# Kernel optimization log

Hardware: AMD Instinct MI355X
Metric: run time of the kernel (lower is better)

## Reference

```python
import jax, jax.numpy as jnp
import numpy as np

B, X, Y, Z = 2, 64, 64, 48
T_IN, T_OUT = 10, 20
WIDTH = 20
G = 4              # number of fields / groups
M1 = M2 = M3 = 8   # fourier modes
L = 4              # layers
ORDER = [[0, 1, 2, 3], [1, 2, 3, 0], [2, 3, 0, 1], [3, 0, 1, 2]]
CIN = WIDTH * 4    # mWidth_input_parameters[i] == 4
COUT = WIDTH       # nWidth_output_parameters[i] == 1
EPS = 1e-5


def setup_inputs() -> dict:
    key = jax.random.key(0)
    ks = jax.random.split(key, 12)
    s = 0.02
    return {
        "x": jax.random.normal(ks[0], (B, X, Y, Z, G * T_IN), jnp.float32),
        "p_w": jax.random.normal(ks[1], (G, T_IN + 3, WIDTH), jnp.float32) * s,
        "p_b": jnp.zeros((G, WIDTH), jnp.float32),
        # complex spectral weights stored as (..., 2) = (real, imag); 4 corner blocks
        "spec_w": jax.random.normal(ks[2], (L, G, 4, CIN, COUT, M1, M2, M3, 2), jnp.float32) * (1.0 / CIN),
        "mlp_w1": jax.random.normal(ks[3], (L, G, COUT, COUT), jnp.float32) * s,
        "mlp_b1": jnp.zeros((L, G, COUT), jnp.float32),
        "mlp_w2": jax.random.normal(ks[4], (L, G, COUT, COUT), jnp.float32) * s,
        "mlp_b2": jnp.zeros((L, G, COUT), jnp.float32),
        "w_w": jax.random.normal(ks[5], (L, G, COUT, CIN), jnp.float32) * s,
        "w_b": jnp.zeros((L, G, COUT), jnp.float32),
        "q_w1": jax.random.normal(ks[6], (G, 4 * COUT, COUT), jnp.float32) * s,
        "q_b1": jnp.zeros((G, 4 * COUT), jnp.float32),
        "q_w2": jax.random.normal(ks[7], (G, T_OUT, 4 * COUT), jnp.float32) * s,
        "q_b2": jnp.zeros((G, T_OUT), jnp.float32),
    }


def _instance_norm(v):  # (B,C,X,Y,Z); InstanceNorm3d, affine=False
    m = v.mean(axis=(-3, -2, -1), keepdims=True)
    var = v.var(axis=(-3, -2, -1), keepdims=True)
    return (v - m) * jax.lax.rsqrt(var + EPS)


def _conv1x1(v, w, b):  # w: (Co, Ci)
    return jnp.einsum('bixyz,oi->boxyz', v, w) + b[None, :, None, None, None]


def _gelu(v):
    return jax.nn.gelu(v, approximate=False)


def _spectral(v, w):  # v: (B,Ci,X,Y,Z); w: complex (4,Ci,Co,M1,M2,M3)
    ft = jnp.fft.rfftn(v, axes=(-3, -2, -1))
    mul = lambda xc, wc: jnp.einsum('bixyz,ioxyz->boxyz', xc, wc)
    out = jnp.zeros((v.shape[0], w.shape[2], X, Y, Z // 2 + 1), ft.dtype)
    out = out.at[:, :, :M1, :M2, :M3].set(mul(ft[:, :, :M1, :M2, :M3], w[0]))
    out = out.at[:, :, -M1:, :M2, :M3].set(mul(ft[:, :, -M1:, :M2, :M3], w[1]))
    out = out.at[:, :, :M1, -M2:, :M3].set(mul(ft[:, :, :M1, -M2:, :M3], w[2]))
    out = out.at[:, :, -M1:, -M2:, :M3].set(mul(ft[:, :, -M1:, -M2:, :M3], w[3]))
    return jnp.fft.irfftn(out, s=(X, Y, Z), axes=(-3, -2, -1))


def _grid():  # (1,X,Y,Z,3), linspace 0..1 per axis
    gx = jnp.linspace(0.0, 1.0, X, dtype=jnp.float32)[:, None, None]
    gy = jnp.linspace(0.0, 1.0, Y, dtype=jnp.float32)[None, :, None]
    gz = jnp.linspace(0.0, 1.0, Z, dtype=jnp.float32)[None, None, :]
    g = jnp.stack([jnp.broadcast_to(gx, (X, Y, Z)),
                   jnp.broadcast_to(gy, (X, Y, Z)),
                   jnp.broadcast_to(gz, (X, Y, Z))], axis=-1)
    return g[None]


def reference(x, p_w, p_b, spec_w, mlp_w1, mlp_b1, mlp_w2, mlp_b2,
              w_w, w_b, q_w1, q_b1, q_w2, q_b2):
    grid = jnp.broadcast_to(_grid(), (x.shape[0], X, Y, Z, 3))
    # --- lifting: per-field Linear(T_in+3 -> width) ---
    lifted = [jnp.concatenate([x[..., i * T_IN:(i + 1) * T_IN], grid], axis=-1) @ p_w[i] + p_b[i]
              for i in range(G)]
    h = jnp.concatenate(lifted, axis=-1).transpose(0, 4, 1, 2, 3)  # (B, width*G, X, Y, Z)
    sw = spec_w[..., 0] + 1j * spec_w[..., 1]
    for l in range(L):
        for i in range(G):
            # faithful gather quirk: first index duplicated, last index dropped
            idx = [ORDER[i][0]] + ORDER[i][:-1]
            xg = jnp.concatenate([h[:, WIDTH * k:WIDTH * (k + 1)] for k in idx], axis=1)
            v = _instance_norm(xg)
            v = _spectral(v, sw[l, i])
            v = _instance_norm(v)
            v = _conv1x1(_gelu(_conv1x1(v, mlp_w1[l, i], mlp_b1[l, i])), mlp_w2[l, i], mlp_b2[l, i])
            r = _conv1x1(xg, w_w[l, i], w_b[l, i])
            h = h.at[:, WIDTH * i:WIDTH * (i + 1)].set(v + r)
        if l != L - 1:
            h = _gelu(h)
    # --- projection: per-field MLP (T_OUT == WIDTH so slices align to field blocks) ---
    outs = []
    for i in range(G):
        lo = (WIDTH if i == 0 else T_OUT) * i
        xi = h[:, lo:lo + WIDTH]
        xi = _conv1x1(_gelu(_conv1x1(xi, q_w1[i], q_b1[i])), q_w2[i], q_b2[i])
        outs.append(xi)
    out = jnp.concatenate(outs, axis=1)
    return out.transpose(0, 2, 3, 4, 1)  # (B,X,Y,Z,G*T_OUT)
```

## Files before the change

### kernel.cpp

```cpp
#include <hip/hip_runtime.h>
#include <math.h>

#define SPAT 196608
#define EPSV 1e-5f

__device__ __forceinline__ float geluf(float x){
    float ax = fabsf(x)*0.70710678118654752440f;
    float t = __builtin_amdgcn_rcpf(1.0f + 0.3275911f*ax);
    float p = ((((1.061405429f*t - 1.453152027f)*t + 1.421413741f)*t - 0.284496736f)*t + 0.254829592f)*t;
    float e = 1.0f - p*__expf(-ax*ax);
    float er = copysignf(e, x);
    return 0.5f*x*(1.0f + er);
}
__device__ __forceinline__ float wred(float v){
    #pragma unroll
    for(int o=32;o>0;o>>=1) v += __shfl_down(v,o);
    return v;
}

__global__ void k_tables(float* tab){
    for(int idx=threadIdx.x; idx<384; idx+=blockDim.x){
        int z = idx>>3, k = idx&7;
        double a = 6.283185307179586476925286766559 * (double)((k*z)%48) / 48.0;
        float c = (float)cos(a), s = (float)sin(a);
        tab[idx]=c; tab[384+idx]=s;
        tab[768 + k*48+z]=c; tab[1152 + k*48+z]=s;
    }
    for(int idx=threadIdx.x; idx<1024; idx+=blockDim.x){
        int y = idx>>4, ki = idx&15;
        int ka = ki<8 ? ki : ki+48;
        double a = 6.283185307179586476925286766559 * (double)((ka*y)%64) / 64.0;
        float c=(float)cos(a), s=(float)sin(a);
        tab[1536+idx]=c; tab[2560+idx]=s;
        tab[3584 + ki*64+y]=c; tab[4608 + ki*64+y]=s;
    }
}

__global__ void __launch_bounds__(256) k_lift(const float* __restrict__ x,
                       const float* __restrict__ pw, const float* __restrict__ pb,
                       float* __restrict__ h){
    int t = blockIdx.x*256 + threadIdx.x;
    int b = (t>=SPAT) ? 1 : 0; int col = t - b*SPAT;
    int xy = col/48, z = col%48;
    const float4* xp = (const float4*)(x + (size_t)t*40);
    float in[40];
    #pragma unroll
    for(int q=0;q<10;q++){
        float4 v = xp[q];
        in[q*4]=v.x; in[q*4+1]=v.y; in[q*4+2]=v.z; in[q*4+3]=v.w;
    }
    float gx = (float)(xy>>6)*(1.0f/63.0f);
    float gy = (float)(xy&63)*(1.0f/63.0f);
    float gz = (float)z*(1.0f/47.0f);
    for(int g=0;g<4;g++){
        const float* w = pw + g*260;
        #pragma unroll 4
        for(int c=0;c<20;c++){
            float a = pb[g*20+c];
            #pragma unroll
            for(int j=0;j<10;j++) a += in[g*10+j]*w[j*20+c];
            a += gx*w[200+c] + gy*w[220+c] + gz*w[240+c];
            h[(size_t)(b*80+g*20+c)*SPAT + col] = a;
        }
    }
}

__global__ void __launch_bounds__(256) k_zy(const float* __restrict__ h,
        float* __restrict__ ybuf, float* __restrict__ partZY,
        const float* __restrict__ tab, int gA,int gB,int gC,int gD, int gflag){
    __shared__ float sp4[4*16*65];
    __shared__ float cyl[16*65], syl[16*65];
    __shared__ float sred[8];
    int blk = blockIdx.x;
    int x = blk&63; int d=(blk>>6)%20; int r2 = blk/1280; int b = r2&1; int gi = r2>>1;
    int gl4[4]={gA,gB,gC,gD};
    int g = gl4[gi];
    int ch = g*20+d;
    int tid=threadIdx.x;
    int y = tid&63, q4 = tid>>6;
    const float4* src = (const float4*)(h + (size_t)(b*80+ch)*SPAT + (size_t)x*3072
                                          + (size_t)(y*48 + q4*12));
    float v[12];
    #pragma unroll
    for(int u=0;u<3;u++){
        float4 t4 = src[u];
        v[u*4]=t4.x; v[u*4+1]=t4.y; v[u*4+2]=t4.z; v[u*4+3]=t4.w;
    }
    if(gflag){
        #pragma unroll
        for(int j=0;j<12;j++) v[j]=geluf(v[j]);
    }
    float s1=0,s2=0;
    #pragma unroll
    for(int j=0;j<12;j++){ s1+=v[j]; s2+=v[j]*v[j]; }
    for(int tt=tid;tt<1024;tt+=256){
        int ki=tt>>6, yy=tt&63;
        cyl[ki*65+yy]=tab[3584+tt]; syl[ki*65+yy]=tab[4608+tt];
    }
    const float* CZ = tab+768  + q4*12;
    const float* SZ = tab+1152 + q4*12;
    #pragma unroll
    for(int k=0;k<8;k++){
        float rr=0, si=0;
        #pragma unroll
        for(int j=0;j<12;j++){ rr += v[j]*CZ[k*48+j]; si += v[j]*SZ[k*48+j]; }
        sp4[(q4*16 + k*2)*65 + y]   = rr;
        sp4[(q4*16 + k*2+1)*65 + y] = -si;
    }
    s1=wred(s1); s2=wred(s2);
    if((tid&63)==0){ sred[(tid>>6)*2]=s1; sred[(tid>>6)*2+1]=s2; }
    __syncthreads();
    if(tid==0){
        size_t pi = ((size_t)(b*80+ch)*64+x)*2;
        partZY[pi]   = sred[0]+sred[2]+sred[4]+sred[6];
        partZY[pi+1] = sred[1]+sred[3]+sred[5]+sred[7];
    }
    #pragma unroll
    for(int j=0;j<4;j++){
        int e = tid + j*256;
        int kri = e>>6, yy = e&63;
        float sum = sp4[kri*65+yy] + sp4[(16+kri)*65+yy]
                  + sp4[(32+kri)*65+yy] + sp4[(48+kri)*65+yy];
        sp4[kri*65+yy] = sum;
    }
    __syncthreads();
    if(tid<128){
        int ky=tid>>3, kz=tid&7;
        const float* cy = cyl+ky*65; const float* sy = syl+ky*65;
        const float* spr = sp4 + (kz*2)*65;
        const float* spi = sp4 + (kz*2+1)*65;
        float fr=0, fi=0;
        #pragma unroll 8
        for(int yy=0;yy<64;yy++){
            float sr=spr[yy], si=spi[yy];
            float c=cy[yy], s=sy[yy];
            fr += sr*c + si*s;
            fi += si*c - sr*s;
        }
        size_t base = ((size_t)((g*2+b)*20+d)*16 + ky)*1024 + (size_t)(kz*128);
        ybuf[base + x]      = fr;
        ybuf[base + 64 + x] = fi;
    }
}

__global__ void __launch_bounds__(128) k_xdft(const float* __restrict__ ybuf,
        float* __restrict__ fbufC, const float* __restrict__ partZY,
        const float* __restrict__ tab, int gA,int gB,int gC,int gD){
    __shared__ __align__(16) float ylx[16*68];
    __shared__ float cxl[16*65], sxl[16*65];
    __shared__ float scs[1];
    int blk = blockIdx.x;
    int kyi = blk&15; int d=(blk>>4)%20; int r2=blk/320; int b=r2&1; int gi=r2>>1;
    int gl4[4]={gA,gB,gC,gD};
    int g=gl4[gi]; int ch=g*20+d;
    int tid=threadIdx.x;
    const float4* src = (const float4*)(ybuf + (((size_t)((g*2+b)*20+d)*16+kyi)*1024));
    #pragma unroll
    for(int u=0;u<2;u++){
        int e=tid+u*128; float4 v=src[e];
        int kzri = e>>4; int xx=(e&15)*4;
        *(float4*)(ylx + kzri*68 + xx) = v;
    }
    for(int tt=tid;tt<1024;tt+=128){
        int ki=tt>>6, y=tt&63;
        cxl[ki*65+y]=tab[3584+tt]; sxl[ki*65+y]=tab[4608+tt];
    }
    float s1=0,s2=0;
    if(tid<64){
        size_t pi=((size_t)(b*80+ch)*64+tid)*2;
        s1=partZY[pi]; s2=partZY[pi+1];
    }
    s1=wred(s1); s2=wred(s2);
    if(tid==0){
        float mean=s1*(1.0f/196608.0f);
        float var=s2*(1.0f/196608.0f)-mean*mean;
        scs[0]=rsqrtf(var+EPSV);
    }
    __syncthreads();
    float sc = scs[0];
    int kxi=tid>>3, kz=tid&7;
    const float* yr = ylx + (kz*2)*68;
    const float* yi = ylx + (kz*2+1)*68;
    const float* cx = cxl + kxi*65;
    const float* sx = sxl + kxi*65;
    float fr=0, fi=0;
    #pragma unroll 8
    for(int xx=0;xx<64;xx++){
        float a=yr[xx], e2=yi[xx];
        float c=cx[xx], s=sx[xx];
        fr += a*c + e2*s;
        fi += e2*c - a*s;
    }
    fr*=sc; fi*=sc;
    if(kxi==0 && kyi==0 && kz==0){ fr=0.0f; fi=0.0f; }
    size_t idx = ((size_t)(b*80+ch)*2048 + (size_t)((kxi*16+kyi)*8+kz))*2;
    fbufC[idx]=fr; fbufC[idx+1]=fi;
}

__global__ void __launch_bounds__(256) k_spec(const float* __restrict__ fbufC,
        const float* __restrict__ sw, float* __restrict__ gbuf,
        float* __restrict__ stat2, int li, int g0, int g1, int g2){
    __shared__ float part[2112];
    int blk = blockIdx.x;
    int m1p = blk & 3, o = (blk>>2)%20, q = blk/80;
    int tid = threadIdx.x;
    int t64 = tid & 63, cc = tid >> 6;
    if(q==0 && m1p==0 && tid<2){
        stat2[(tid*20+o)*2]=0.f; stat2[(tid*20+o)*2+1]=0.f;
    }
    int offx = (q&1)*8, offy = (q>>1)*8;
    int m1 = m1p*2 + (t64>>5);
    int m2 = (t64>>2)&7;
    int m3 = (t64&3)*2;
    int tw = m1*64 + m2*8 + m3;
    int kxi = m1+offx, kyi = m2+offy;
    int fo = (kxi*16 + kyi)*8 + m3;
    const float4* wp = (const float4*)(sw + (((size_t)(li*4+q)*1600) + o)*1024 + (size_t)tw*2);
    const float4* fb = (const float4*)fbufC + (fo>>1);
    float r00=0,i00=0,r01=0,i01=0, r10=0,i10=0,r11=0,i11=0;
    int c0 = cc*5;
    #pragma unroll
    for(int u=0;u<5;u++){
        int c = c0+u;
        float4 wa = wp[(size_t)c*5120];
        float4 wb4= wp[(size_t)(c+20)*5120];
        float wr0 = wa.x + wb4.x, wi0 = wa.y + wb4.y, wr1 = wa.z + wb4.z, wi1 = wa.w + wb4.w;
        float4 f0 = fb[(size_t)(g0*20+c)*1024];
        float4 f1 = fb[(size_t)(80+g0*20+c)*1024];
        r00 += f0.x*wr0 - f0.y*wi0; i00 += f0.x*wi0 + f0.y*wr0;
        r01 += f0.z*wr1 - f0.w*wi1; i01 += f0.z*wi1 + f0.w*wr1;
        r10 += f1.x*wr0 - f1.y*wi0; i10 += f1.x*wi0 + f1.y*wr0;
        r11 += f1.z*wr1 - f1.w*wi1; i11 += f1.z*wi1 + f1.w*wr1;
    }
    #pragma unroll
    for(int u=0;u<5;u++){
        int c = c0+u;
        float4 wa = wp[(size_t)(c+40)*5120];
        float4 f0 = fb[(size_t)(g1*20+c)*1024];
        float4 f1 = fb[(size_t)(80+g1*20+c)*1024];
        r00 += f0.x*wa.x - f0.y*wa.y; i00 += f0.x*wa.y + f0.y*wa.x;
        r01 += f0.z*wa.z - f0.w*wa.w; i01 += f0.z*wa.w + f0.w*wa.z;
        r10 += f1.x*wa.x - f1.y*wa.y; i10 += f1.x*wa.y + f1.y*wa.x;
        r11 += f1.z*wa.z - f1.w*wa.w; i11 += f1.z*wa.w + f1.w*wa.z;
    }
    #pragma unroll
    for(int u=0;u<5;u++){
        int c = c0+u;
        float4 wa = wp[(size_t)(c+60)*5120];
        float4 f0 = fb[(size_t)(g2*20+c)*1024];
        float4 f1 = fb[(size_t)(80+g2*20+c)*1024];
        r00 += f0.x*wa.x - f0.y*wa.y; i00 += f0.x*wa.y + f0.y*wa.x;
        r01 += f0.z*wa.z - f0.w*wa.w; i01 += f0.z*wa.w + f0.w*wa.z;
        r10 += f1.x*wa.x - f1.y*wa.y; i10 += f1.x*wa.y + f1.y*wa.x;
        r11 += f1.z*wa.z - f1.w*wa.w; i11 += f1.z*wa.w + f1.w*wa.z;
    }
    float vals[8]={r00,i00,r01,i01,r10,i10,r11,i11};
    #pragma unroll
    for(int e=0;e<8;e++) part[t64*33 + e*4 + cc] = vals[e];
    __syncthreads();
    if(cc==0){
        float acc[8];
        #pragma unroll
        for(int e=0;e<8;e++){
            const float* p = part + t64*33 + e*4;
            acc[e] = p[0]+p[1]+p[2]+p[3];
        }
        float4* gg0 = (float4*)(gbuf + (size_t)o*4096 + fo*2);
        float4* gg1 = (float4*)(gbuf + (size_t)(20+o)*4096 + fo*2);
        *gg0 = make_float4(acc[0],acc[1],acc[2],acc[3]);
        *gg1 = make_float4(acc[4],acc[5],acc[6],acc[7]);
    }
}

__global__ void k_inv(const float* __restrict__ gbuf, float* __restrict__ iybuf,
                      float* __restrict__ stat2, const float* __restrict__ tab){
    __shared__ __align__(16) float gl[4096];
    __shared__ float tmp[256];
    __shared__ float cl[1088], sl[1088];
    __shared__ float ig[4];
    int blk = blockIdx.x;
    int nx = blk&63, o = (blk>>6)%20, b = blk/1280;
    const float4* src4 = (const float4*)(gbuf + (size_t)(b*20+o)*4096);
    for(int t=threadIdx.x;t<1024;t+=blockDim.x) ((float4*)gl)[t]=src4[t];
    for(int t=threadIdx.x;t<1024;t+=blockDim.x){
        int y=t>>4, ki=t&15;
        cl[y*17+ki]=tab[1536+t]; sl[y*17+ki]=tab[2560+t];
    }
    __syncthreads();
    {
        int kyi = threadIdx.x>>3, kz = threadIdx.x&7;
        float ar=0, ai=0;
        #pragma unroll 4
        for(int kxi=0;kxi<16;kxi++){
            float gr = gl[((kxi*16+kyi)*8+kz)*2], gi2 = gl[((kxi*16+kyi)*8+kz)*2+1];
            float c = cl[nx*17+kxi], s = sl[nx*17+kxi];
            ar += gr*c - gi2*s;
            ai += gi2*c + gr*s;
        }
        tmp[threadIdx.x*2]   = ar*(1.0f/64.0f);
        tmp[threadIdx.x*2+1] = ai*(1.0f/64.0f);
    }
    __syncthreads();
    float p1=0,p2=0;
    for(int j=0;j<4;j++){
        int out = threadIdx.x + j*128;
        int ny = out>>3, kz = out&7;
        float ar=0, ai=0;
        #pragma unroll 4
        for(int kyi=0;kyi<16;kyi++){
            float vr = tmp[(kyi*8+kz)*2], vi = tmp[(kyi*8+kz)*2+1];
            float c = cl[ny*17+kyi], s = sl[ny*17+kyi];
            ar += vr*c - vi*s;
            ai += vi*c + vr*s;
        }
        ar *= (1.0f/64.0f); ai *= (1.0f/64.0f);
        size_t idx = ((((size_t)(b*20+o)*64+nx)*64+ny)*8+kz)*2;
        iybuf[idx]=ar; iybuf[idx+1]=ai;
        if(kz==0){ p1 += ar; p2 += ar*ar; }
        else p2 += 2.0f*(ar*ar+ai*ai);
    }
    p2 *= (1.0f/48.0f);
    float r1=wred(p1), r2=wred(p2);
    int wv = threadIdx.x>>6;
    if((threadIdx.x&63)==0){ ig[wv*2]=r1; ig[wv*2+1]=r2; }
    __syncthreads();
    if(threadIdx.x==0){
        atomicAdd(&stat2[(b*20+o)*2],   ig[0]+ig[2]);
        atomicAdd(&stat2[(b*20+o)*2+1], ig[1]+ig[3]);
    }
}

__global__ void __launch_bounds__(256) k_passD(
        const float* __restrict__ iybuf,
        const float* __restrict__ w1, const float* __restrict__ b1,
        const float* __restrict__ w2, const float* __restrict__ b2,
        const float* __restrict__ ww, const float* __restrict__ wb,
        float* __restrict__ h,
        const float* __restrict__ stat2, const float* __restrict__ tab,
        int li, int grp, int g1, int g2, int f0, int f1, int f2){
    __shared__ __align__(16) float dl[2560];
    __shared__ float m2l[20], s2l[20];
    __shared__ float czl[384], szl[384];
    int blk = blockIdx.x;
    int nyt = blk&7, nx=(blk>>3)&63, b = blk>>9;
    int tid = threadIdx.x;
    for(int u=tid; u<640; u+=256){
        int o = u>>5, j = u&31;
        const float4* s4 = (const float4*)(iybuf + ((((size_t)(b*20+o)*64+nx)*64 + nyt*8)*16));
        ((float4*)dl)[o*32+j] = s4[j];
    }
    if(tid<20){
        float S1 = stat2[(b*20+tid)*2], S2 = stat2[(b*20+tid)*2+1];
        float mean = S1*(1.0f/196608.0f);
        float var = S2*(1.0f/196608.0f) - mean*mean;
        m2l[tid]=mean; s2l[tid]=rsqrtf(var+EPSV);
    }
    for(int t=tid;t<384;t+=256){ czl[t]=tab[768+t]; szl[t]=tab[1152+t]; }
    __syncthreads();
    if(tid>=192) return;
    int p0 = tid*2;
    int nyl = p0/48, nz0 = p0 - nyl*48;
    float vj0[20], vj1[20];
    #pragma unroll
    for(int o=0;o<20;o++){
        const float* dd = dl + o*128 + nyl*16;
        float a0 = dd[0], a1 = dd[0];
        #pragma unroll
        for(int k=1;k<8;k++){
            float dr = dd[k*2], di = dd[k*2+1];
            a0 += 2.0f*(dr*czl[k*48+nz0]   - di*szl[k*48+nz0]);
            a1 += 2.0f*(dr*czl[k*48+nz0+1] - di*szl[k*48+nz0+1]);
        }
        vj0[o] = (a0*(1.0f/48.0f) - m2l[o])*s2l[o];
        vj1[o] = (a1*(1.0f/48.0f) - m2l[o])*s2l[o];
    }
    const float* W1 = w1 + li*400; const float* W2 = w2 + li*400;
    const float* B1 = b1 + li*20;  const float* B2 = b2 + li*20;
    float t10[20], t11[20];
    #pragma unroll
    for(int oo=0;oo<20;oo++){
        float a0=B1[oo], a1=a0;
        #pragma unroll
        for(int j=0;j<20;j++){ float w=W1[oo*20+j]; a0+=vj0[j]*w; a1+=vj1[j]*w; }
        t10[oo]=geluf(a0); t11[oo]=geluf(a1);
    }
    float o0[20], o1[20];
    #pragma unroll
    for(int oo=0;oo<20;oo++){
        float a0=B2[oo], a1=a0;
        #pragma unroll
        for(int j=0;j<20;j++){ float w=W2[oo*20+j]; a0+=t10[j]*w; a1+=t11[j]*w; }
        o0[oo]=a0; o1[oo]=a1;
    }
    int sb = (nx*64 + nyt*8)*48;
    const float* W = ww + li*1600;
    const float* hb = h + (size_t)(b*80)*SPAT + sb + p0;
    #pragma unroll
    for(int o=0;o<20;o++){ float bv=wb[li*20+o]; o0[o]+=bv; o1[o]+=bv; }
    for(int c=0;c<20;c++){
        float2 vv = *(const float2*)(hb + (size_t)(grp*20+c)*SPAT);
        if(f0){ vv.x=geluf(vv.x); vv.y=geluf(vv.y); }
        #pragma unroll
        for(int o=0;o<20;o++){
            float w = W[o*80+c] + W[o*80+20+c];
            o0[o]+=w*vv.x; o1[o]+=w*vv.y;
        }
    }
    for(int c=0;c<20;c++){
        float2 vv = *(const float2*)(hb + (size_t)(g1*20+c)*SPAT);
        if(f1){ vv.x=geluf(vv.x); vv.y=geluf(vv.y); }
        #pragma unroll
        for(int o=0;o<20;o++){
            float w = W[o*80+40+c];
            o0[o]+=w*vv.x; o1[o]+=w*vv.y;
        }
    }
    for(int c=0;c<20;c++){
        float2 vv = *(const float2*)(hb + (size_t)(g2*20+c)*SPAT);
        if(f2){ vv.x=geluf(vv.x); vv.y=geluf(vv.y); }
        #pragma unroll
        for(int o=0;o<20;o++){
            float w = W[o*80+60+c];
            o0[o]+=w*vv.x; o1[o]+=w*vv.y;
        }
    }
    #pragma unroll
    for(int o=0;o<20;o++)
        *(float2*)(h + (size_t)(b*80+grp*20+o)*SPAT + sb + p0) = make_float2(o0[o],o1[o]);
}

__global__ void __launch_bounds__(256) k_head(const float* __restrict__ h,
        const float* __restrict__ qw1, const float* __restrict__ qb1,
        const float* __restrict__ qw2, const float* __restrict__ qb2,
        float* __restrict__ out){
    int g = blockIdx.x & 3;
    int t = (blockIdx.x>>2)*256 + threadIdx.x;
    if(t >= 196608) return;
    int b = (t>=98304) ? 1 : 0; int col = (t - b*98304)*2;
    const float* hb = h + (size_t)(b*80+g*20)*SPAT + col;
    float2 in20[20];
    #pragma unroll
    for(int j=0;j<20;j++) in20[j] = *(const float2*)(hb + (size_t)j*SPAT);
    float2 o20[20];
    #pragma unroll
    for(int o2=0;o2<20;o2++){ float bv = qb2[g*20+o2]; o20[o2].x=bv; o20[o2].y=bv; }
    for(int o8=0;o8<80;o8++){
        float bv = qb1[g*80+o8];
        float a0 = bv, a1 = bv;
        #pragma unroll
        for(int j=0;j<20;j++){
            float w = qw1[g*1600 + o8*20 + j];
            a0 += in20[j].x*w; a1 += in20[j].y*w;
        }
        a0 = geluf(a0); a1 = geluf(a1);
        #pragma unroll
        for(int o2=0;o2<20;o2++){
            float w = qw2[g*1600 + o2*80 + o8];
            o20[o2].x += a0*w; o20[o2].y += a1*w;
        }
    }
    float* op0 = out + ((size_t)(b*SPAT)+col)*80 + g*20;
    float* op1 = op0 + 80;
    #pragma unroll
    for(int q2=0;q2<5;q2++){
        *(float4*)(op0 + q2*4) = make_float4(o20[q2*4].x,o20[q2*4+1].x,o20[q2*4+2].x,o20[q2*4+3].x);
        *(float4*)(op1 + q2*4) = make_float4(o20[q2*4].y,o20[q2*4+1].y,o20[q2*4+2].y,o20[q2*4+3].y);
    }
}

extern "C" void kernel_launch(void* const* d_in, const int* in_sizes, int n_in,
                              void* d_out, int out_size, void* d_ws, size_t ws_size,
                              hipStream_t stream){
    (void)in_sizes; (void)n_in; (void)out_size;
    const float* x    = (const float*)d_in[0];
    const float* p_w  = (const float*)d_in[1];
    const float* p_b  = (const float*)d_in[2];
    const float* spec = (const float*)d_in[3];
    const float* w1   = (const float*)d_in[4];
    const float* b1   = (const float*)d_in[5];
    const float* w2   = (const float*)d_in[6];
    const float* b2   = (const float*)d_in[7];
    const float* ww   = (const float*)d_in[8];
    const float* wb   = (const float*)d_in[9];
    const float* qw1  = (const float*)d_in[10];
    const float* qb1  = (const float*)d_in[11];
    const float* qw2  = (const float*)d_in[12];
    const float* qb2  = (const float*)d_in[13];
    float* out = (float*)d_out;
    float* ws  = (float*)d_ws;

    if(ws_size < (size_t)37545552*4) return;

    float* h      = ws;
    float* ybuf   = ws + 31457280;
    float* gbuf   = ws + 34078720;
    float* iyb    = ws + 34242560;
    float* fbufC  = ws + 36864000;
    float* partZY = ws + 37519360;
    float* stat2  = ws + 37539840;
    float* tab    = ws + 37539920;

    k_tables<<<1,256,0,stream>>>(tab);
    k_lift<<<1536,256,0,stream>>>(x, p_w, p_b, h);

    static const int ORD3[4][3] = {{0,1,2},{1,2,3},{2,3,0},{3,0,1}};
    for(int l=0;l<4;l++){
        int lf = (l>0)?1:0;
        for(int bi=0;bi<2;bi++){
            if(bi==0){
                k_zy  <<<10240,256,0,stream>>>(h, ybuf, partZY, tab, 0,1,2,3, lf);
                k_xdft<<< 2560,128,0,stream>>>(ybuf, fbufC, partZY, tab, 0,1,2,3);
            } else {
                k_zy  <<< 5120,256,0,stream>>>(h, ybuf, partZY, tab, 0,1,0,0, 0);
                k_xdft<<< 1280,128,0,stream>>>(ybuf, fbufC, partZY, tab, 0,1,0,0);
            }
            for(int ii=0;ii<2;ii++){
                int i = bi*2+ii; int li = l*4+i;
                int g0=ORD3[i][0], g1=ORD3[i][1], g2=ORD3[i][2];
                (void)g0;
                int f0 = lf;
                int f1 = (g1<i)?0:lf;
                int f2 = (g2<i)?0:lf;
                k_spec <<< 320,256,0,stream>>>(fbufC, spec, gbuf, stat2, li, i, g1, g2);
                k_inv  <<<2560,128,0,stream>>>(gbuf, iyb, stat2, tab);
                k_passD<<<1024,256,0,stream>>>(iyb, w1, b1, w2, b2, ww, wb, h, stat2, tab,
                                               li, i, g1, g2, f0, f1, f2);
            }
        }
    }
    k_head<<<3072,256,0,stream>>>(h, qw1, qb1, qw2, qb2, out);
}
```

Measured before the change: 3.269 ms.

## Batch two field groups per spectral, inverse and pointwise pass

The spectral-multiply, inverse-DFT and pointwise MLP/residual kernels now each handle two independent field groups in a single launch instead of two. Workspace buffers for gbuf, iybuf and stats are doubled and indexed by group. The fused pointwise kernel reads each input field block of h once and feeds both groups' residual convolutions, which cuts repeated global reads and launch count. The cost is much higher register pressure from four 20-wide accumulator arrays plus larger shared memory, which may lower occupancy or cause spills.

```diff
diff --git a/kernel.cpp b/kernel.cpp
--- a/kernel.cpp
+++ b/kernel.cpp
@@ -197,16 +197,22 @@
     fbufC[idx]=fr; fbufC[idx+1]=fi;
 }
 
-__global__ void __launch_bounds__(256) k_spec(const float* __restrict__ fbufC,
+__global__ void __launch_bounds__(256) k_spec2(const float* __restrict__ fbufC,
         const float* __restrict__ sw, float* __restrict__ gbuf,
-        float* __restrict__ stat2, int li, int g0, int g1, int g2){
+        float* __restrict__ stat2, int li0,
+        int i0, int gA1, int gA2, int i1, int gB1, int gB2){
     __shared__ float part[2112];
     int blk = blockIdx.x;
-    int m1p = blk & 3, o = (blk>>2)%20, q = blk/80;
+    int it = blk/320; int r = blk - it*320;
+    int m1p = r & 3, o = (r>>2)%20, q = r/80;
+    int li = li0 + it;
+    int g0 = it ? i1 : i0;
+    int g1 = it ? gB1 : gA1;
+    int g2 = it ? gB2 : gA2;
     int tid = threadIdx.x;
     int t64 = tid & 63, cc = tid >> 6;
     if(q==0 && m1p==0 && tid<2){
-        stat2[(tid*20+o)*2]=0.f; stat2[(tid*20+o)*2+1]=0.f;
+        stat2[((it*2+tid)*20+o)*2]=0.f; stat2[((it*2+tid)*20+o)*2+1]=0.f;
     }
     int offx = (q&1)*8, offy = (q>>1)*8;
     int m1 = m1p*2 + (t64>>5);
@@ -265,22 +271,24 @@
             const float* p = part + t64*33 + e*4;
             acc[e] = p[0]+p[1]+p[2]+p[3];
         }
-        float4* gg0 = (float4*)(gbuf + (size_t)o*4096 + fo*2);
-        float4* gg1 = (float4*)(gbuf + (size_t)(20+o)*4096 + fo*2);
+        float* gb = gbuf + (size_t)it*163840;
+        float4* gg0 = (float4*)(gb + (size_t)o*4096 + fo*2);
+        float4* gg1 = (float4*)(gb + (size_t)(20+o)*4096 + fo*2);
         *gg0 = make_float4(acc[0],acc[1],acc[2],acc[3]);
         *gg1 = make_float4(acc[4],acc[5],acc[6],acc[7]);
     }
 }
 
-__global__ void k_inv(const float* __restrict__ gbuf, float* __restrict__ iybuf,
-                      float* __restrict__ stat2, const float* __restrict__ tab){
+__global__ void k_inv2(const float* __restrict__ gbuf, float* __restrict__ iybuf,
+                       float* __restrict__ stat2, const float* __restrict__ tab){
     __shared__ __align__(16) float gl[4096];
     __shared__ float tmp[256];
     __shared__ float cl[1088], sl[1088];
     __shared__ float ig[4];
     int blk = blockIdx.x;
-    int nx = blk&63, o = (blk>>6)%20, b = blk/1280;
-    const float4* src4 = (const float4*)(gbuf + (size_t)(b*20+o)*4096);
+    int it = blk/2560; int r = blk - it*2560;
+    int nx = r&63, o = (r>>6)%20, b = r/1280;
+    const float4* src4 = (const float4*)(gbuf + (size_t)it*163840 + (size_t)(b*20+o)*4096);
     for(int t=threadIdx.x;t<1024;t+=blockDim.x) ((float4*)gl)[t]=src4[t];
     for(int t=threadIdx.x;t<1024;t+=blockDim.x){
         int y=t>>4, ki=t&15;
@@ -314,7 +322,7 @@
             ai += vi*c + vr*s;
         }
         ar *= (1.0f/64.0f); ai *= (1.0f/64.0f);
-        size_t idx = ((((size_t)(b*20+o)*64+nx)*64+ny)*8+kz)*2;
+        size_t idx = ((((size_t)((it*2+b)*20+o)*64+nx)*64+ny)*8+kz)*2;
         iybuf[idx]=ar; iybuf[idx+1]=ai;
         if(kz==0){ p1 += ar; p2 += ar*ar; }
         else p2 += 2.0f*(ar*ar+ai*ai);
@@ -325,108 +333,152 @@
     if((threadIdx.x&63)==0){ ig[wv*2]=r1; ig[wv*2+1]=r2; }
     __syncthreads();
     if(threadIdx.x==0){
-        atomicAdd(&stat2[(b*20+o)*2],   ig[0]+ig[2]);
-        atomicAdd(&stat2[(b*20+o)*2+1], ig[1]+ig[3]);
-    }
-}
-
-__global__ void __launch_bounds__(256) k_passD(
+        atomicAdd(&stat2[((it*2+b)*20+o)*2],   ig[0]+ig[2]);
+        atomicAdd(&stat2[((it*2+b)*20+o)*2+1], ig[1]+ig[3]);
+    }
+}
+
+__global__ void __launch_bounds__(256) k_passD2(
         const float* __restrict__ iybuf,
         const float* __restrict__ w1, const float* __restrict__ b1,
         const float* __restrict__ w2, const float* __restrict__ b2,
         const float* __restrict__ ww, const float* __restrict__ wb,
         float* __restrict__ h,
         const float* __restrict__ stat2, const float* __restrict__ tab,
-        int li, int grp, int g1, int g2, int f0, int f1, int f2){
-    __shared__ __align__(16) float dl[2560];
-    __shared__ float m2l[20], s2l[20];
+        int li0, int i0, int i1, int gA1, int gA2, int gB1, int gB2,
+        int fl0, int fl1, int fl2, int fl3){
+    __shared__ __align__(16) float dl[5120];
+    __shared__ float m2l[2][20], s2l[2][20];
     __shared__ float czl[384], szl[384];
     int blk = blockIdx.x;
     int nyt = blk&7, nx=(blk>>3)&63, b = blk>>9;
     int tid = threadIdx.x;
-    for(int u=tid; u<640; u+=256){
-        int o = u>>5, j = u&31;
-        const float4* s4 = (const float4*)(iybuf + ((((size_t)(b*20+o)*64+nx)*64 + nyt*8)*16));
-        ((float4*)dl)[o*32+j] = s4[j];
-    }
-    if(tid<20){
-        float S1 = stat2[(b*20+tid)*2], S2 = stat2[(b*20+tid)*2+1];
+    for(int u=tid; u<1280; u+=256){
+        int itu = (u>=640)?1:0; int rem = u - itu*640;
+        int o = rem>>5, j = rem&31;
+        const float4* s4 = (const float4*)(iybuf +
+            ((((size_t)((itu*2+b)*20+o)*64+nx)*64 + nyt*8)*16));
+        ((float4*)dl)[itu*640 + o*32 + j] = s4[j];
+    }
+    if(tid<40){
+        int itq = tid/20, oq = tid - itq*20;
+        float S1 = stat2[((itq*2+b)*20+oq)*2], S2 = stat2[((itq*2+b)*20+oq)*2+1];
         float mean = S1*(1.0f/196608.0f);
         float var = S2*(1.0f/196608.0f) - mean*mean;
-        m2l[tid]=mean; s2l[tid]=rsqrtf(var+EPSV);
+        m2l[itq][oq]=mean; s2l[itq][oq]=rsqrtf(var+EPSV);
     }
     for(int t=tid;t<384;t+=256){ czl[t]=tab[768+t]; szl[t]=tab[1152+t]; }
     __syncthreads();
     if(tid>=192) return;
     int p0 = tid*2;
     int nyl = p0/48, nz0 = p0 - nyl*48;
-    float vj0[20], vj1[20];
+    float oA0[20], oA1[20], oB0[20], oB1[20];
+    {
+        float vj0[20], vj1[20];
+        #pragma unroll
+        for(int o=0;o<20;o++){
+            const float* dd = dl + o*128 + nyl*16;
+            float a0 = dd[0], a1 = dd[0];
+            #pragma unroll
+            for(int k=1;k<8;k++){
+                float dr = dd[k*2], di = dd[k*2+1];
+                a0 += 2.0f*(dr*czl[k*48+nz0]   - di*szl[k*48+nz0]);
+                a1 += 2.0f*(dr*czl[k*48+nz0+1] - di*szl[k*48+nz0+1]);
+            }
+            vj0[o] = (a0*(1.0f/48.0f) - m2l[0][o])*s2l[0][o];
+            vj1[o] = (a1*(1.0f/48.0f) - m2l[0][o])*s2l[0][o];
+        }
+        const float* W1 = w1 + li0*400; const float* W2 = w2 + li0*400;
+        const float* B1 = b1 + li0*20;  const float* B2 = b2 + li0*20;
+        float t10[20], t11[20];
+        #pragma unroll
+        for(int oo=0;oo<20;oo++){
+            float a0=B1[oo], a1=a0;
+            #pragma unroll
+            for(int j=0;j<20;j++){ float w=W1[oo*20+j]; a0+=vj0[j]*w; a1+=vj1[j]*w; }
+            t10[oo]=geluf(a0); t11[oo]=geluf(a1);
+        }
+        #pragma unroll
+        for(int oo=0;oo<20;oo++){
+            float bb = B2[oo] + wb[li0*20+oo];
+            float a0=bb, a1=bb;
+            #pragma unroll
+            for(int j=0;j<20;j++){ float w=W2[oo*20+j]; a0+=t10[j]*w; a1+=t11[j]*w; }
+            oA0[oo]=a0; oA1[oo]=a1;
+        }
+    }
+    {
+        int li1 = li0+1;
+        float vj0[20], vj1[20];
+        #pragma unroll
+        for(int o=0;o<20;o++){
+            const float* dd = dl + 2560 + o*128 + nyl*16;
+            float a0 = dd[0], a1 = dd[0];
+            #pragma unroll
+            for(int k=1;k<8;k++){
+                float dr = dd[k*2], di = dd[k*2+1];
+                a0 += 2.0f*(dr*czl[k*48+nz0]   - di*szl[k*48+nz0]);
+                a1 += 2.0f*(dr*czl[k*48+nz0+1] - di*szl[k*48+nz0+1]);
+            }
+            vj0[o] = (a0*(1.0f/48.0f) - m2l[1][o])*s2l[1][o];
+            vj1[o] = (a1*(1.0f/48.0f) - m2l[1][o])*s2l[1][o];
+        }
+        const float* W1 = w1 + li1*400; const float* W2 = w2 + li1*400;
+        const float* B1 = b1 + li1*20;  const float* B2 = b2 + li1*20;
+        float t10[20], t11[20];
+        #pragma unroll
+        for(int oo=0;oo<20;oo++){
+            float a0=B1[oo], a1=a0;
+            #pragma unroll
+            for(int j=0;j<20;j++){ float w=W1[oo*20+j]; a0+=vj0[j]*w; a1+=vj1[j]*w; }
+            t10[oo]=geluf(a0); t11[oo]=geluf(a1);
+        }
+        #pragma unroll
+        for(int oo=0;oo<20;oo++){
+            float bb = B2[oo] + wb[li1*20+oo];
+            float a0=bb, a1=bb;
+            #pragma unroll
+            for(int j=0;j<20;j++){ float w=W2[oo*20+j]; a0+=t10[j]*w; a1+=t11[j]*w; }
+            oB0[oo]=a0; oB1[oo]=a1;
+        }
+    }
+    int sb = (nx*64 + nyt*8)*48;
+    const float* hb = h + (size_t)(b*80)*SPAT + sb + p0;
+    const float* WA = ww + li0*1600;
+    const float* WB = ww + (li0+1)*1600;
+    #pragma unroll
+    for(int g=0; g<4; g++){
+        int flag = (g==0)?fl0:((g==1)?fl1:((g==2)?fl2:fl3));
+        for(int c=0;c<20;c++){
+            float2 vv = *(const float2*)(hb + (size_t)(g*20+c)*SPAT);
+            if(flag){ vv.x=geluf(vv.x); vv.y=geluf(vv.y); }
+            if(g==i0){
+                #pragma unroll
+                for(int o=0;o<20;o++){ float w = WA[o*80+c]+WA[o*80+20+c]; oA0[o]+=w*vv.x; oA1[o]+=w*vv.y; }
+            } else if(g==gA1){
+                #pragma unroll
+                for(int o=0;o<20;o++){ float w = WA[o*80+40+c]; oA0[o]+=w*vv.x; oA1[o]+=w*vv.y; }
+            } else if(g==gA2){
+                #pragma unroll
+                for(int o=0;o<20;o++){ float w = WA[o*80+60+c]; oA0[o]+=w*vv.x; oA1[o]+=w*vv.y; }
+            }
+            if(g==i1){
+                #pragma unroll
+                for(int o=0;o<20;o++){ float w = WB[o*80+c]+WB[o*80+20+c]; oB0[o]+=w*vv.x; oB1[o]+=w*vv.y; }
+            } else if(g==gB1){
+                #pragma unroll
+                for(int o=0;o<20;o++){ float w = WB[o*80+40+c]; oB0[o]+=w*vv.x; oB1[o]+=w*vv.y; }
+            } else if(g==gB2){
+                #pragma unroll
+                for(int o=0;o<20;o++){ float w = WB[o*80+60+c]; oB0[o]+=w*vv.x; oB1[o]+=w*vv.y; }
+            }
+        }
+    }
     #pragma unroll
     for(int o=0;o<20;o++){
-        const float* dd = dl + o*128 + nyl*16;
-        float a0 = dd[0], a1 = dd[0];
-        #pragma unroll
-        for(int k=1;k<8;k++){
-            float dr = dd[k*2], di = dd[k*2+1];
-            a0 += 2.0f*(dr*czl[k*48+nz0]   - di*szl[k*48+nz0]);
-            a1 += 2.0f*(dr*czl[k*48+nz0+1] - di*szl[k*48+nz0+1]);
-        }
-        vj0[o] = (a0*(1.0f/48.0f) - m2l[o])*s2l[o];
-        vj1[o] = (a1*(1.0f/48.0f) - m2l[o])*s2l[o];
-    }
-    const float* W1 = w1 + li*400; const float* W2 = w2 + li*400;
-    const float* B1 = b1 + li*20;  const float* B2 = b2 + li*20;
-    float t10[20], t11[20];
-    #pragma unroll
-    for(int oo=0;oo<20;oo++){
-        float a0=B1[oo], a1=a0;
-        #pragma unroll
-        for(int j=0;j<20;j++){ float w=W1[oo*20+j]; a0+=vj0[j]*w; a1+=vj1[j]*w; }
-        t10[oo]=geluf(a0); t11[oo]=geluf(a1);
-    }
-    float o0[20], o1[20];
-    #pragma unroll
-    for(int oo=0;oo<20;oo++){
-        float a0=B2[oo], a1=a0;
-        #pragma unroll
-        for(int j=0;j<20;j++){ float w=W2[oo*20+j]; a0+=t10[j]*w; a1+=t11[j]*w; }
-        o0[oo]=a0; o1[oo]=a1;
-    }
-    int sb = (nx*64 + nyt*8)*48;
-    const float* W = ww + li*1600;
-    const float* hb = h + (size_t)(b*80)*SPAT + sb + p0;
-    #pragma unroll
-    for(int o=0;o<20;o++){ float bv=wb[li*20+o]; o0[o]+=bv; o1[o]+=bv; }
-    for(int c=0;c<20;c++){
-        float2 vv = *(const float2*)(hb + (size_t)(grp*20+c)*SPAT);
-        if(f0){ vv.x=geluf(vv.x); vv.y=geluf(vv.y); }
-        #pragma unroll
-        for(int o=0;o<20;o++){
-            float w = W[o*80+c] + W[o*80+20+c];
-            o0[o]+=w*vv.x; o1[o]+=w*vv.y;
-        }
-    }
-    for(int c=0;c<20;c++){
-        float2 vv = *(const float2*)(hb + (size_t)(g1*20+c)*SPAT);
-        if(f1){ vv.x=geluf(vv.x); vv.y=geluf(vv.y); }
-        #pragma unroll
-        for(int o=0;o<20;o++){
-            float w = W[o*80+40+c];
-            o0[o]+=w*vv.x; o1[o]+=w*vv.y;
-        }
-    }
-    for(int c=0;c<20;c++){
-        float2 vv = *(const float2*)(hb + (size_t)(g2*20+c)*SPAT);
-        if(f2){ vv.x=geluf(vv.x); vv.y=geluf(vv.y); }
-        #pragma unroll
-        for(int o=0;o<20;o++){
-            float w = W[o*80+60+c];
-            o0[o]+=w*vv.x; o1[o]+=w*vv.y;
-        }
-    }
-    #pragma unroll
-    for(int o=0;o<20;o++)
-        *(float2*)(h + (size_t)(b*80+grp*20+o)*SPAT + sb + p0) = make_float2(o0[o],o1[o]);
+        *(float2*)(h + (size_t)(b*80+i0*20+o)*SPAT + sb + p0) = make_float2(oA0[o],oA1[o]);
+        *(float2*)(h + (size_t)(b*80+i1*20+o)*SPAT + sb + p0) = make_float2(oB0[o],oB1[o]);
+    }
 }
 
 __global__ void __launch_bounds__(256) k_head(const float* __restrict__ h,
@@ -489,16 +541,16 @@
     float* out = (float*)d_out;
     float* ws  = (float*)d_ws;
 
-    if(ws_size < (size_t)37545552*4) return;
+    if(ws_size < (size_t)40330912*4) return;
 
     float* h      = ws;
     float* ybuf   = ws + 31457280;
     float* gbuf   = ws + 34078720;
-    float* iyb    = ws + 34242560;
-    float* fbufC  = ws + 36864000;
-    float* partZY = ws + 37519360;
-    float* stat2  = ws + 37539840;
-    float* tab    = ws + 37539920;
+    float* iyb    = ws + 34406400;
+    float* fbufC  = ws + 39649280;
+    float* partZY = ws + 40304640;
+    float* stat2  = ws + 40325120;
+    float* tab    = ws + 40325280;
 
     k_tables<<<1,256,0,stream>>>(tab);
     k_lift<<<1536,256,0,stream>>>(x, p_w, p_b, h);
@@ -514,18 +566,17 @@
                 k_zy  <<< 5120,256,0,stream>>>(h, ybuf, partZY, tab, 0,1,0,0, 0);
                 k_xdft<<< 1280,128,0,stream>>>(ybuf, fbufC, partZY, tab, 0,1,0,0);
             }
-            for(int ii=0;ii<2;ii++){
-                int i = bi*2+ii; int li = l*4+i;
-                int g0=ORD3[i][0], g1=ORD3[i][1], g2=ORD3[i][2];
-                (void)g0;
-                int f0 = lf;
-                int f1 = (g1<i)?0:lf;
-                int f2 = (g2<i)?0:lf;
-                k_spec <<< 320,256,0,stream>>>(fbufC, spec, gbuf, stat2, li, i, g1, g2);
-                k_inv  <<<2560,128,0,stream>>>(gbuf, iyb, stat2, tab);
-                k_passD<<<1024,256,0,stream>>>(iyb, w1, b1, w2, b2, ww, wb, h, stat2, tab,
-                                               li, i, g1, g2, f0, f1, f2);
-            }
+            int i0 = bi*2, i1 = i0+1, li0 = l*4+i0;
+            int gA1=ORD3[i0][1], gA2=ORD3[i0][2];
+            int gB1=ORD3[i1][1], gB2=ORD3[i1][2];
+            k_spec2<<< 640,256,0,stream>>>(fbufC, spec, gbuf, stat2, li0,
+                                           i0,gA1,gA2, i1,gB1,gB2);
+            k_inv2 <<<5120,128,0,stream>>>(gbuf, iyb, stat2, tab);
+            int f0,f1,f2,f3;
+            if(bi==0){ f0=lf; f1=lf; f2=lf; f3=lf; }
+            else     { f0=0;  f1=0;  f2=lf; f3=lf; }
+            k_passD2<<<1024,256,0,stream>>>(iyb, w1,b1,w2,b2, ww,wb, h, stat2, tab,
+                                            li0, i0,i1, gA1,gA2, gB1,gB2, f0,f1,f2,f3);
         }
     }
     k_head<<<3072,256,0,stream>>>(h, qw1, qb1, qw2, qb2, out);
```

Result: slower. 5.646 ms (+72.7%).
